# Optimization experiments

Measured on AMD Instinct MI355X. Metric: run time of the kernel, lower is better.

## Reference

```python
import jax, jax.numpy as jnp
import numpy as np

NU = 500000   # num user nodes
NI = 100000   # num item nodes
F  = 300      # item feature dim
D  = 64       # hidden channels
E  = 2000000  # num rated edges
EL = 1000000  # num supervision (label) edges


def setup_inputs() -> dict:
    key = jax.random.key(0)
    ks = jax.random.split(key, 24)
    def nrm(k, shp, scale=0.05):
        return jax.random.normal(k, shp, dtype=jnp.float32) * scale
    inp = {
        "user_emb_w": nrm(ks[0], (NU, D)),
        "item_x": jax.random.normal(ks[1], (NI, F), dtype=jnp.float32),
        "item_lin_w": nrm(ks[2], (F, D)),
        "item_lin_b": jnp.zeros((D,), jnp.float32),
        "Wl1_ui": nrm(ks[3], (D, D)), "Wr1_ui": nrm(ks[4], (D, D)), "b1_ui": jnp.zeros((D,), jnp.float32),
        "Wl1_iu": nrm(ks[5], (D, D)), "Wr1_iu": nrm(ks[6], (D, D)), "b1_iu": jnp.zeros((D,), jnp.float32),
        "Wl2_ui": nrm(ks[7], (D, D)), "Wr2_ui": nrm(ks[8], (D, D)), "b2_ui": jnp.zeros((D,), jnp.float32),
        "Wl2_iu": nrm(ks[9], (D, D)), "Wr2_iu": nrm(ks[10], (D, D)), "b2_iu": jnp.zeros((D,), jnp.float32),
        "user_node_id": jnp.arange(NU, dtype=jnp.int32),
        "edge_src": jax.random.randint(ks[11], (E,), 0, NU, dtype=jnp.int32),
        "edge_dst": jax.random.randint(ks[12], (E,), 0, NI, dtype=jnp.int32),
        "label_src": jax.random.randint(ks[13], (EL,), 0, NU, dtype=jnp.int32),
        "label_dst": jax.random.randint(ks[14], (EL,), 0, NI, dtype=jnp.int32),
    }
    return inp


def _seg_mean(x_src, src, dst, n_dst):
    # mean-aggregate source features onto destination nodes (PyG SAGEConv aggr='mean')
    s = jax.ops.segment_sum(x_src[src], dst, num_segments=n_dst)
    c = jax.ops.segment_sum(jnp.ones(src.shape, x_src.dtype), dst, num_segments=n_dst)
    return s / jnp.maximum(c, 1.0)[:, None]


def reference(user_emb_w, item_x, item_lin_w, item_lin_b,
              Wl1_ui, Wr1_ui, b1_ui, Wl1_iu, Wr1_iu, b1_iu,
              Wl2_ui, Wr2_ui, b2_ui, Wl2_iu, Wr2_iu, b2_iu,
              user_node_id, edge_src, edge_dst, label_src, label_dst):
    # input layers: user embedding lookup, item linear projection
    x_user = user_emb_w[user_node_id]                 # [NU, D]
    x_item = item_x @ item_lin_w + item_lin_b         # [NI, D]

    def hetero_sage(xu, xi, Wl_ui, Wr_ui, bui, Wl_iu, Wr_iu, biu):
        # edge type (user, rates, item): aggregate user msgs at items
        hi = _seg_mean(xu, edge_src, edge_dst, NI) @ Wl_ui + bui + xi @ Wr_ui
        # edge type (item, rev_rates, user): aggregate item msgs at users
        hu = _seg_mean(xi, edge_dst, edge_src, NU) @ Wl_iu + biu + xu @ Wr_iu
        return hu, hi

    hu, hi = hetero_sage(x_user, x_item, Wl1_ui, Wr1_ui, b1_ui, Wl1_iu, Wr1_iu, b1_iu)
    hu, hi = jax.nn.relu(hu), jax.nn.relu(hi)
    hu, hi = hetero_sage(hu, hi, Wl2_ui, Wr2_ui, b2_ui, Wl2_iu, Wr2_iu, b2_iu)

    # DOT predictor on edge_label_index pairs
    return jnp.sum(hu[label_src] * hi[label_dst], axis=-1)   # [EL]
```

## Files before the change

kernel.cpp:

```cpp
#include <hip/hip_runtime.h>

#define NUu 500000
#define NIi 100000
#define FDIM 300
#define DDIM 64
#define NEe 2000000
#define ELl 1000000
#define EMAX (NEe - 1)

#define BSZL_I 8
#define BSZL_U 9
#define NB_I 391
#define NB_U 977
#define NBT (NB_I + NB_U)
#define SH_I 19
#define SH_U 17

typedef __attribute__((ext_vector_type(8))) short s8v;
typedef __attribute__((ext_vector_type(4))) short s4v;
typedef __attribute__((ext_vector_type(4))) float f4v;
typedef unsigned short u16;

__device__ __forceinline__ float bf2f(u16 h) {
    union { unsigned u; float f; } x; x.u = ((unsigned)h) << 16; return x.f;
}
__device__ __forceinline__ u16 f2bf(float f) {
    union { float f; unsigned u; } x; x.f = f;
    unsigned u = x.u;
    u += 0x7FFFu + ((u >> 16) & 1u);
    return (u16)(u >> 16);
}

__global__ __launch_bounds__(256) void k_cast_users(const float* __restrict__ ue,
                                                    const int* __restrict__ uid,
                                                    u16* __restrict__ xu) {
    int idx = blockIdx.x * 256 + threadIdx.x;
    int n  = idx >> 4;
    int d0 = (idx & 15) * 4;
    int src = uid[n];
    const float4* p = (const float4*)(ue + (size_t)src * DDIM + d0);
    float4 v = *p;
    s4v o;
    o[0] = (short)f2bf(v.x); o[1] = (short)f2bf(v.y);
    o[2] = (short)f2bf(v.z); o[3] = (short)f2bf(v.w);
    *(s4v*)(xu + (size_t)n * DDIM + d0) = o;
}

__global__ __launch_bounds__(256) void k_cast_w(const float* __restrict__ W,
                                                u16* __restrict__ wbf) {
    int idx = blockIdx.x * 256 + threadIdx.x;
    if (idx >= 2560) return;
    int f = idx >> 6, lane = idx & 63;
    int q = lane >> 4, c = lane & 15;
    int kstep = f >> 2, nb = f & 3;
    u16* dst = wbf + (size_t)idx * 8;
#pragma unroll
    for (int j = 0; j < 8; j++) {
        int k = kstep * 32 + q * 8 + j;
        float v = (k < FDIM) ? W[k * DDIM + nb * 16 + c] : 0.f;
        dst[j] = f2bf(v);
    }
}

__global__ __launch_bounds__(256) void k_cast_w8(
    const float* __restrict__ W0, const float* __restrict__ W1,
    const float* __restrict__ W2, const float* __restrict__ W3,
    const float* __restrict__ W4, const float* __restrict__ W5,
    const float* __restrict__ W6, const float* __restrict__ W7,
    u16* __restrict__ out) {
    int idx = blockIdx.x * 256 + threadIdx.x;
    if (idx >= 4096) return;
    int wm = idx >> 9;
    int s = idx & 511;
    int ks = s >> 8, nb = (s >> 6) & 3, lane = s & 63;
    int q = lane >> 4, c = lane & 15;
    const float* W;
    switch (wm) {
        case 0: W = W0; break; case 1: W = W1; break;
        case 2: W = W2; break; case 3: W = W3; break;
        case 4: W = W4; break; case 5: W = W5; break;
        case 6: W = W6; break; default: W = W7; break;
    }
    u16* dst = out + (size_t)idx * 8;
#pragma unroll
    for (int j = 0; j < 8; j++) {
        int row = ks * 32 + q * 8 + j;
        dst[j] = f2bf(W[row * DDIM + nb * 16 + c]);
    }
}

__global__ __launch_bounds__(256) void k_item_lin2(const float* __restrict__ ix,
                                                   const u16* __restrict__ wbf,
                                                   const float* __restrict__ b,
                                                   u16* __restrict__ xi) {
    __shared__ __align__(16) u16 wl[40 * 64 * 8];
    int tid = threadIdx.x;
    for (int i = tid; i < 2560; i += 256)
        ((f4v*)wl)[i] = ((const f4v*)wbf)[i];
    __syncthreads();

    int lane = tid & 63;
    int q = lane >> 4, c = lane & 15;
    float bv[4];
#pragma unroll
    for (int nb = 0; nb < 4; nb++) bv[nb] = b[nb * 16 + c];

    int w = blockIdx.x * 4 + (tid >> 6);
    int stride = gridDim.x * 4;
    const int NT = NIi / 16;
    for (int t = w; t < NT; t += stride) {
        int row = t * 16 + c;
        const float* xr = ix + (size_t)row * FDIM;
        f4v acc[4];
#pragma unroll
        for (int nb = 0; nb < 4; nb++) {
            acc[nb][0] = bv[nb]; acc[nb][1] = bv[nb];
            acc[nb][2] = bv[nb]; acc[nb][3] = bv[nb];
        }
#pragma unroll
        for (int ks = 0; ks < 10; ks++) {
            s8v a;
            if (ks < 9 || q == 0) {
                float4 v0 = *(const float4*)(xr + ks * 32 + q * 8);
                float4 v1 = *(const float4*)(xr + ks * 32 + q * 8 + 4);
                a[0] = (short)f2bf(v0.x); a[1] = (short)f2bf(v0.y);
                a[2] = (short)f2bf(v0.z); a[3] = (short)f2bf(v0.w);
                a[4] = (short)f2bf(v1.x); a[5] = (short)f2bf(v1.y);
                a[6] = (short)f2bf(v1.z); a[7] = (short)f2bf(v1.w);
            } else {
                float4 v0 = *(const float4*)(xr + 296);
                a[0] = (short)f2bf(v0.x); a[1] = (short)f2bf(v0.y);
                a[2] = (short)f2bf(v0.z); a[3] = (short)f2bf(v0.w);
                a[4] = 0; a[5] = 0; a[6] = 0; a[7] = 0;
            }
#pragma unroll
            for (int nb = 0; nb < 4; nb++) {
                s8v bb = *(const s8v*)(wl + ((size_t)(ks * 4 + nb) * 64 + lane) * 8);
                acc[nb] = __builtin_amdgcn_mfma_f32_16x16x32_bf16(a, bb, acc[nb], 0, 0, 0);
            }
        }
#pragma unroll
        for (int nb = 0; nb < 4; nb++)
#pragma unroll
            for (int r = 0; r < 4; r++)
                xi[(size_t)(t * 16 + q * 4 + r) * DDIM + nb * 16 + c] = f2bf(acc[nb][r]);
    }
}

__global__ __launch_bounds__(256) void k_hist(const int* __restrict__ src,
                                              const int* __restrict__ dst,
                                              int* __restrict__ hist) {
    __shared__ int h[NBT];
    int t = threadIdx.x;
    for (int c = t; c < NBT; c += 256) h[c] = 0;
    __syncthreads();
    int base = blockIdx.x * 2048;
#pragma unroll
    for (int k = 0; k < 8; k++) {
        int e = base + k * 256 + t;
        if (e < NEe) {
            int s = src[e], d = dst[e];
            atomicAdd(&h[d >> BSZL_I], 1);
            atomicAdd(&h[NB_I + (s >> BSZL_U)], 1);
        }
    }
    __syncthreads();
    for (int c = t; c < NBT; c += 256) {
        int n = h[c];
        if (n) atomicAdd(&hist[c], n);
    }
}

__device__ __forceinline__ void scanN(const int* __restrict__ cnt, int n, int total,
                                      int* __restrict__ base, int* __restrict__ frontier,
                                      int* sb) {
    int t = threadIdx.x;
    int v[8]; int s = 0;
#pragma unroll
    for (int i = 0; i < 8; i++) {
        int idx = t * 8 + i;
        v[i] = (idx < n) ? cnt[idx] : 0;
        s += v[i];
    }
    sb[t] = s; __syncthreads();
    for (int o = 1; o < 256; o <<= 1) {
        int a = (t >= o) ? sb[t - o] : 0;
        __syncthreads();
        sb[t] += a;
        __syncthreads();
    }
    int run = sb[t] - s;
#pragma unroll
    for (int i = 0; i < 8; i++) {
        int idx = t * 8 + i;
        if (idx < n) { base[idx] = run; frontier[idx] = run; }
        run += v[i];
    }
    if (t == 0) base[n] = total;
    __syncthreads();
}

__global__ __launch_bounds__(256) void k_bucket_scan(const int* __restrict__ hist,
                                                     int* __restrict__ base_i, int* __restrict__ fr_i,
                                                     int* __restrict__ base_u, int* __restrict__ fr_u,
                                                     int* __restrict__ rpi, int* __restrict__ rpu) {
    __shared__ int sb[256];
    scanN(hist, NB_I, NEe, base_i, fr_i, sb);
    scanN(hist + NB_I, NB_U, NEe, base_u, fr_u, sb);
    if (threadIdx.x == 0) { rpi[NIi] = NEe; rpu[NUu] = NEe; }
}

__global__ __launch_bounds__(256) void k_scatter(const int* __restrict__ src,
                                                 const int* __restrict__ dst,
                                                 int* __restrict__ fr_i, int* __restrict__ fr_u,
                                                 unsigned* __restrict__ scat_i,
                                                 unsigned* __restrict__ scat_u) {
    __shared__ int h[NBT];
    int t = threadIdx.x;
    for (int c = t; c < NBT; c += 256) h[c] = 0;
    __syncthreads();
    int base = blockIdx.x * 2048;
#pragma unroll
    for (int k = 0; k < 8; k++) {
        int e = base + k * 256 + t;
        if (e < NEe) {
            int s = src[e], d = dst[e];
            atomicAdd(&h[d >> BSZL_I], 1);
            atomicAdd(&h[NB_I + (s >> BSZL_U)], 1);
        }
    }
    __syncthreads();
    for (int c = t; c < NBT; c += 256) {
        int n = h[c];
        if (n) {
            int b = (c < NB_I) ? atomicAdd(&fr_i[c], n) : atomicAdd(&fr_u[c - NB_I], n);
            h[c] = b;
        }
    }
    __syncthreads();
#pragma unroll
    for (int k = 0; k < 8; k++) {
        int e = base + k * 256 + t;
        if (e < NEe) {
            int s = src[e], d = dst[e];
            int p = atomicAdd(&h[d >> BSZL_I], 1);
            scat_i[p] = (unsigned)s | ((unsigned)(d & 255) << SH_I);
            int q = atomicAdd(&h[NB_I + (s >> BSZL_U)], 1);
            scat_u[q] = (unsigned)d | ((unsigned)(s & 511) << SH_U);
        }
    }
}

__global__ __launch_bounds__(256) void k_bfill(const unsigned* __restrict__ scat,
                                               const int* __restrict__ base,
                                               int* __restrict__ rp, int* __restrict__ col,
                                               int shift, int bszlog, int ntotal) {
    __shared__ int cnt[512];
    __shared__ int pos[512];
    __shared__ int sb[256];
    int b = blockIdx.x;
    int t = threadIdx.x;
    int e0 = base[b], e1 = base[b + 1];
    int node0 = b << bszlog;
    int bsz = 1 << bszlog;
    unsigned mask = (1u << shift) - 1u;

    for (int c = t; c < bsz; c += 256) cnt[c] = 0;
    __syncthreads();
    for (int e = e0 + t; e < e1; e += 256) {
        unsigned v = scat[e];
        atomicAdd(&cnt[v >> shift], 1);
    }
    __syncthreads();
    int per = bsz >> 8;
    int loc[2]; int ls = 0;
#pragma unroll
    for (int i = 0; i < 2; i++) {
        loc[i] = (i < per) ? cnt[t * per + i] : 0;
        ls += loc[i];
    }
    sb[t] = ls; __syncthreads();
    for (int o = 1; o < 256; o <<= 1) {
        int a = (t >= o) ? sb[t - o] : 0;
        __syncthreads();
        sb[t] += a;
        __syncthreads();
    }
    int run = e0 + sb[t] - ls;
#pragma unroll
    for (int i = 0; i < 2; i++) {
        if (i < per) {
            int idx = t * per + i;
            int node = node0 + idx;
            if (node < ntotal) rp[node] = run;
            pos[idx] = run;
            run += loc[i];
        }
    }
    __syncthreads();
    for (int e = e0 + t; e < e1; e += 256) {
        unsigned v = scat[e];
        int l = v >> shift;
        int p = atomicAdd(&pos[l], 1);
        col[p] = (int)(v & mask);
    }
}

__global__ __launch_bounds__(256) void k_fused(const u16* __restrict__ feat,
                                               const u16* __restrict__ xf,
                                               const u16* __restrict__ wfrag,
                                               const float* __restrict__ bias,
                                               u16* __restrict__ out,
                                               const int* __restrict__ rp,
                                               const int* __restrict__ col,
                                               int ntiles, int relu) {
    __shared__ __align__(16) u16 wsh[8192];
    int tid = threadIdx.x;
    for (int i = tid; i < 1024; i += 256)
        ((f4v*)wsh)[i] = ((const f4v*)wfrag)[i];
    __syncthreads();

    int lane = tid & 63;
    int q = lane >> 4, c = lane & 15;
    int w = blockIdx.x * 4 + (tid >> 6);
    int stride = gridDim.x * 4;
    float bv[4];
#pragma unroll
    for (int nb = 0; nb < 4; nb++) bv[nb] = bias[nb * 16 + c];

    for (int t = w; t < ntiles; t += stride) {
        int node = t * 16 + c;
        int s0 = rp[node], s1 = rp[node + 1];
        int deg = s1 - s0;
        float inv = (deg > 0) ? 1.0f / (float)deg : 0.0f;

        const s8v* px = (const s8v*)(xf + (size_t)node * DDIM + q * 8);
        s8v x0 = px[0], x1 = px[4];

        float accA[8] = {0.f, 0.f, 0.f, 0.f, 0.f, 0.f, 0.f, 0.f};
        float accB[8] = {0.f, 0.f, 0.f, 0.f, 0.f, 0.f, 0.f, 0.f};

        for (int i = 0; __any(i < deg); i += 2) {
            int ia = s0 + i;
            int ea = min(ia, EMAX);
            int eb = min(ia + 1, EMAX);
            int ra = col[ea];
            int rb = col[eb];
            float ma = (i < deg) ? inv : 0.f;
            float mb = (i + 1 < deg) ? inv : 0.f;
            const u16* fa = feat + (size_t)ra * DDIM + q * 8;
            const u16* fb = feat + (size_t)rb * DDIM + q * 8;
            s8v va0 = *(const s8v*)fa;
            s8v va1 = *(const s8v*)(fa + 32);
            s8v vb0 = *(const s8v*)fb;
            s8v vb1 = *(const s8v*)(fb + 32);
#pragma unroll
            for (int j = 0; j < 8; j++) {
                accA[j] = fmaf(ma, bf2f((u16)va0[j]), accA[j]);
                accB[j] = fmaf(ma, bf2f((u16)va1[j]), accB[j]);
                accA[j] = fmaf(mb, bf2f((u16)vb0[j]), accA[j]);
                accB[j] = fmaf(mb, bf2f((u16)vb1[j]), accB[j]);
            }
        }

        s8v a0, a1;
#pragma unroll
        for (int j = 0; j < 8; j++) {
            a0[j] = (short)f2bf(accA[j]);
            a1[j] = (short)f2bf(accB[j]);
        }

        f4v acc[4];
#pragma unroll
        for (int nb = 0; nb < 4; nb++) {
            acc[nb][0] = bv[nb]; acc[nb][1] = bv[nb];
            acc[nb][2] = bv[nb]; acc[nb][3] = bv[nb];
        }

        unsigned lz = (unsigned)lane * 8u;
        asm volatile("" : "+v"(lz));
        const u16* wb = wsh + lz;
#pragma unroll
        for (int nb = 0; nb < 4; nb++) {
            s8v wl0 = *(const s8v*)(wb + nb * 512);
            s8v wl1 = *(const s8v*)(wb + 2048 + nb * 512);
            s8v wr0 = *(const s8v*)(wb + 4096 + nb * 512);
            s8v wr1 = *(const s8v*)(wb + 6144 + nb * 512);
            acc[nb] = __builtin_amdgcn_mfma_f32_16x16x32_bf16(a0, wl0, acc[nb], 0, 0, 0);
            acc[nb] = __builtin_amdgcn_mfma_f32_16x16x32_bf16(a1, wl1, acc[nb], 0, 0, 0);
            acc[nb] = __builtin_amdgcn_mfma_f32_16x16x32_bf16(x0, wr0, acc[nb], 0, 0, 0);
            acc[nb] = __builtin_amdgcn_mfma_f32_16x16x32_bf16(x1, wr1, acc[nb], 0, 0, 0);
        }
#pragma unroll
        for (int nb = 0; nb < 4; nb++)
#pragma unroll
            for (int r = 0; r < 4; r++) {
                float v = acc[nb][r];
                if (relu) v = fmaxf(v, 0.f);
                out[(size_t)(t * 16 + q * 4 + r) * DDIM + nb * 16 + c] = f2bf(v);
            }
    }
}

__global__ __launch_bounds__(256) void k_dot(const u16* __restrict__ hu,
                                             const u16* __restrict__ hi,
                                             const int* __restrict__ ls,
                                             const int* __restrict__ ld,
                                             float* __restrict__ out) {
    int lane = threadIdx.x & 63;
    int sub = lane >> 3, t8 = lane & 7;
    int w = blockIdx.x * 4 + (threadIdx.x >> 6);
    int stride = gridDim.x * 4;
    const int ngroups = ELl / 8;
    for (int g = w; g < ngroups; g += stride) {
        int e = g * 8 + sub;
        int u = ls[e], it = ld[e];
        s8v av = *(const s8v*)(hu + (size_t)u  * DDIM + t8 * 8);
        s8v bv = *(const s8v*)(hi + (size_t)it * DDIM + t8 * 8);
        float s = 0.f;
#pragma unroll
        for (int k = 0; k < 8; k++) s += bf2f((u16)av[k]) * bf2f((u16)bv[k]);
        s += __shfl_xor(s, 4);
        s += __shfl_xor(s, 2);
        s += __shfl_xor(s, 1);
        if (t8 == 0) out[e] = s;
    }
}

extern "C" void kernel_launch(void* const* d_in, const int* in_sizes, int n_in,
                              void* d_out, int out_size, void* d_ws, size_t ws_size,
                              hipStream_t stream) {
    const float* user_emb = (const float*)d_in[0];
    const float* item_x   = (const float*)d_in[1];
    const float* item_w   = (const float*)d_in[2];
    const float* item_b   = (const float*)d_in[3];
    const float* Wl1_ui = (const float*)d_in[4];
    const float* Wr1_ui = (const float*)d_in[5];
    const float* b1_ui  = (const float*)d_in[6];
    const float* Wl1_iu = (const float*)d_in[7];
    const float* Wr1_iu = (const float*)d_in[8];
    const float* b1_iu  = (const float*)d_in[9];
    const float* Wl2_ui = (const float*)d_in[10];
    const float* Wr2_ui = (const float*)d_in[11];
    const float* b2_ui  = (const float*)d_in[12];
    const float* Wl2_iu = (const float*)d_in[13];
    const float* Wr2_iu = (const float*)d_in[14];
    const float* b2_iu  = (const float*)d_in[15];
    const int* uid  = (const int*)d_in[16];
    const int* esrc = (const int*)d_in[17];
    const int* edst = (const int*)d_in[18];
    const int* lsrc = (const int*)d_in[19];
    const int* ldst = (const int*)d_in[20];
    float* out = (float*)d_out;

    char* ws = (char*)d_ws;
    size_t off = 0;
    auto alloc = [&](size_t bytes) -> void* {
        void* p = ws + off;
        off += (bytes + 255) & ~(size_t)255;
        return p;
    };
    u16* xu_b   = (u16*)alloc((size_t)NUu * DDIM * 2);
    u16* hu1_b  = (u16*)alloc((size_t)NUu * DDIM * 2);
    u16* hu2_b  = (u16*)alloc((size_t)NUu * DDIM * 2);
    u16* xi_b   = (u16*)alloc((size_t)NIi * DDIM * 2);
    u16* hi1_b  = (u16*)alloc((size_t)NIi * DDIM * 2);
    u16* hi2_b  = (u16*)alloc((size_t)NIi * DDIM * 2);
    int* coli = (int*)alloc((size_t)NEe * 4);
    int* colu = (int*)alloc((size_t)NEe * 4);
    int* rpi  = (int*)alloc((size_t)(NIi + 1) * 4);
    int* rpu  = (int*)alloc((size_t)(NUu + 1) * 4);
    int* hist   = (int*)alloc((size_t)NBT * 4);
    int* base_i = (int*)alloc((size_t)(NB_I + 1) * 4);
    int* base_u = (int*)alloc((size_t)(NB_U + 1) * 4);
    int* fr_i   = (int*)alloc((size_t)NB_I * 4);
    int* fr_u   = (int*)alloc((size_t)NB_U * 4);
    u16* wbf    = (u16*)alloc((size_t)40 * 64 * 8 * 2);
    u16* wfrag2 = (u16*)alloc((size_t)4 * 8192 * 2);
    unsigned* scat_i = (unsigned*)xu_b;
    unsigned* scat_u = (unsigned*)((char*)xu_b + (size_t)NEe * 4);

    hipMemsetAsync(hist, 0, (size_t)NBT * 4, stream);
    int nchunks = (NEe + 2047) / 2048;
    k_hist<<<nchunks, 256, 0, stream>>>(esrc, edst, hist);
    k_bucket_scan<<<1, 256, 0, stream>>>(hist, base_i, fr_i, base_u, fr_u, rpi, rpu);
    k_scatter<<<nchunks, 256, 0, stream>>>(esrc, edst, fr_i, fr_u, scat_i, scat_u);
    k_bfill<<<NB_I, 256, 0, stream>>>(scat_i, base_i, rpi, coli, SH_I, BSZL_I, NIi);
    k_bfill<<<NB_U, 256, 0, stream>>>(scat_u, base_u, rpu, colu, SH_U, BSZL_U, NUu);

    k_cast_w<<<10, 256, 0, stream>>>(item_w, wbf);
    k_cast_w8<<<16, 256, 0, stream>>>(Wl1_ui, Wr1_ui, Wl1_iu, Wr1_iu,
                                      Wl2_ui, Wr2_ui, Wl2_iu, Wr2_iu, wfrag2);
    k_cast_users<<<NUu * 16 / 256, 256, 0, stream>>>(user_emb, uid, xu_b);
    k_item_lin2<<<512, 256, 0, stream>>>(item_x, wbf, item_b, xi_b);

    const int NT_I = NIi / 16;
    const int NT_U = NUu / 16;

    k_fused<<<512, 256, 0, stream>>>(xu_b, xi_b, wfrag2 + 0 * 8192, b1_ui,
                                     hi1_b, rpi, coli, NT_I, 1);
    k_fused<<<2048, 256, 0, stream>>>(xi_b, xu_b, wfrag2 + 1 * 8192, b1_iu,
                                      hu1_b, rpu, colu, NT_U, 1);
    k_fused<<<512, 256, 0, stream>>>(hu1_b, hi1_b, wfrag2 + 2 * 8192, b2_ui,
                                     hi2_b, rpi, coli, NT_I, 0);
    k_fused<<<2048, 256, 0, stream>>>(hi1_b, hu1_b, wfrag2 + 3 * 8192, b2_iu,
                                      hu2_b, rpu, colu, NT_U, 0);

    k_dot<<<2048, 256, 0, stream>>>(hu2_b, hi2_b, lsrc, ldst, out);
}
```

Baseline: 850.8 us.

## Sort nodes by degree to balance wavefront gather work in fused SAGE kernel

Adds a degree histogram, scan and counting-sort pass so each 16-node tile in the fused aggregation kernel holds nodes of similar degree, reducing divergence in the __any-driven neighbor loop. Outputs are scattered to the original node rows through shuffled node ids. The gather loop is unrolled to four neighbors per iteration with packed bf16 unpacking, and grid sizes for the item kernels are raised. In exchange it adds several small preprocessing kernels, extra index arrays, and non-contiguous stores and self-feature loads.

```diff
diff --git a/kernel.cpp b/kernel.cpp
--- a/kernel.cpp
+++ b/kernel.cpp
@@ -16,9 +16,12 @@
 #define SH_I 19
 #define SH_U 17
 
+#define DBINS 64
+
 typedef __attribute__((ext_vector_type(8))) short s8v;
 typedef __attribute__((ext_vector_type(4))) short s4v;
 typedef __attribute__((ext_vector_type(4))) float f4v;
+typedef __attribute__((ext_vector_type(4))) unsigned u4v;
 typedef unsigned short u16;
 
 __device__ __forceinline__ float bf2f(u16 h) {
@@ -29,6 +32,12 @@
     unsigned u = x.u;
     u += 0x7FFFu + ((u >> 16) & 1u);
     return (u16)(u >> 16);
+}
+__device__ __forceinline__ float lo2f(unsigned u) {
+    union { unsigned x; float f; } c; c.x = u << 16; return c.f;
+}
+__device__ __forceinline__ float hi2f(unsigned u) {
+    union { unsigned x; float f; } c; c.x = u & 0xffff0000u; return c.f;
 }
 
 __global__ __launch_bounds__(256) void k_cast_users(const float* __restrict__ ue,
@@ -306,12 +315,99 @@
     }
 }
 
+__global__ __launch_bounds__(256) void k_dhist(const int* __restrict__ rp,
+                                               int* __restrict__ hist, int n) {
+    __shared__ int h[DBINS];
+    int t = threadIdx.x;
+    if (t < DBINS) h[t] = 0;
+    __syncthreads();
+    int base = blockIdx.x * 2048;
+#pragma unroll
+    for (int k = 0; k < 8; k++) {
+        int i = base + k * 256 + t;
+        if (i < n) {
+            int d = rp[i + 1] - rp[i];
+            atomicAdd(&h[min(d, DBINS - 1)], 1);
+        }
+    }
+    __syncthreads();
+    if (t < DBINS) { int v = h[t]; if (v) atomicAdd(&hist[t], v); }
+}
+
+__global__ void k_dscan2(int* __restrict__ hu, int* __restrict__ hi) {
+    int t = threadIdx.x;
+    int* h = (t < 64) ? hu : hi;
+    int tt = t & 63;
+    int v = h[tt];
+    int s = v;
+#pragma unroll
+    for (int o = 1; o < 64; o <<= 1) {
+        int a = __shfl_up(s, o);
+        if (tt >= o) s += a;
+    }
+    h[tt] = s - v;
+}
+
+__global__ __launch_bounds__(256) void k_dscatter(const int* __restrict__ rp,
+                                                  int* __restrict__ bpos,
+                                                  int* __restrict__ nsort,
+                                                  int* __restrict__ nstart,
+                                                  int* __restrict__ ndeg, int n) {
+    __shared__ int h[DBINS];
+    __shared__ int bb[DBINS];
+    int t = threadIdx.x;
+    if (t < DBINS) h[t] = 0;
+    __syncthreads();
+    int base = blockIdx.x * 2048;
+    int d[8], s0[8];
+#pragma unroll
+    for (int k = 0; k < 8; k++) {
+        int i = base + k * 256 + t;
+        if (i < n) {
+            int a = rp[i], b = rp[i + 1];
+            s0[k] = a;
+            d[k] = b - a;
+            atomicAdd(&h[min(d[k], DBINS - 1)], 1);
+        } else d[k] = -1;
+    }
+    __syncthreads();
+    if (t < DBINS) {
+        int v = h[t];
+        bb[t] = v ? atomicAdd(&bpos[t], v) : 0;
+        h[t] = 0;
+    }
+    __syncthreads();
+#pragma unroll
+    for (int k = 0; k < 8; k++) {
+        if (d[k] >= 0) {
+            int bin = min(d[k], DBINS - 1);
+            int p = bb[bin] + atomicAdd(&h[bin], 1);
+            nsort[p] = base + k * 256 + t;
+            nstart[p] = s0[k];
+            ndeg[p] = d[k];
+        }
+    }
+}
+
+__device__ __forceinline__ void acc_pair(float m, u4v v0, u4v v1,
+                                         float* A, float* B) {
+#pragma unroll
+    for (int k = 0; k < 4; k++) {
+        A[2 * k]     = fmaf(m, lo2f(v0[k]), A[2 * k]);
+        A[2 * k + 1] = fmaf(m, hi2f(v0[k]), A[2 * k + 1]);
+        B[2 * k]     = fmaf(m, lo2f(v1[k]), B[2 * k]);
+        B[2 * k + 1] = fmaf(m, hi2f(v1[k]), B[2 * k + 1]);
+    }
+}
+
 __global__ __launch_bounds__(256) void k_fused(const u16* __restrict__ feat,
                                                const u16* __restrict__ xf,
                                                const u16* __restrict__ wfrag,
                                                const float* __restrict__ bias,
                                                u16* __restrict__ out,
-                                               const int* __restrict__ rp,
+                                               const int* __restrict__ nsort,
+                                               const int* __restrict__ nstart,
+                                               const int* __restrict__ ndeg,
                                                const int* __restrict__ col,
                                                int ntiles, int relu) {
     __shared__ __align__(16) u16 wsh[8192];
@@ -329,9 +425,10 @@
     for (int nb = 0; nb < 4; nb++) bv[nb] = bias[nb * 16 + c];
 
     for (int t = w; t < ntiles; t += stride) {
-        int node = t * 16 + c;
-        int s0 = rp[node], s1 = rp[node + 1];
-        int deg = s1 - s0;
+        int idx = t * 16 + c;
+        int node = nsort[idx];
+        int s0 = nstart[idx];
+        int deg = ndeg[idx];
         float inv = (deg > 0) ? 1.0f / (float)deg : 0.0f;
 
         const s8v* px = (const s8v*)(xf + (size_t)node * DDIM + q * 8);
@@ -340,27 +437,29 @@
         float accA[8] = {0.f, 0.f, 0.f, 0.f, 0.f, 0.f, 0.f, 0.f};
         float accB[8] = {0.f, 0.f, 0.f, 0.f, 0.f, 0.f, 0.f, 0.f};
 
-        for (int i = 0; __any(i < deg); i += 2) {
-            int ia = s0 + i;
-            int ea = min(ia, EMAX);
-            int eb = min(ia + 1, EMAX);
-            int ra = col[ea];
-            int rb = col[eb];
-            float ma = (i < deg) ? inv : 0.f;
-            float mb = (i + 1 < deg) ? inv : 0.f;
-            const u16* fa = feat + (size_t)ra * DDIM + q * 8;
-            const u16* fb = feat + (size_t)rb * DDIM + q * 8;
-            s8v va0 = *(const s8v*)fa;
-            s8v va1 = *(const s8v*)(fa + 32);
-            s8v vb0 = *(const s8v*)fb;
-            s8v vb1 = *(const s8v*)(fb + 32);
-#pragma unroll
-            for (int j = 0; j < 8; j++) {
-                accA[j] = fmaf(ma, bf2f((u16)va0[j]), accA[j]);
-                accB[j] = fmaf(ma, bf2f((u16)va1[j]), accB[j]);
-                accA[j] = fmaf(mb, bf2f((u16)vb0[j]), accA[j]);
-                accB[j] = fmaf(mb, bf2f((u16)vb1[j]), accB[j]);
-            }
+        for (int i = 0; __any(i < deg); i += 4) {
+            int b = s0 + i;
+            int e0 = min(b,     EMAX);
+            int e1 = min(b + 1, EMAX);
+            int e2 = min(b + 2, EMAX);
+            int e3 = min(b + 3, EMAX);
+            int r0 = col[e0], r1 = col[e1], r2 = col[e2], r3 = col[e3];
+            float m0 = (i     < deg) ? inv : 0.f;
+            float m1 = (i + 1 < deg) ? inv : 0.f;
+            float m2 = (i + 2 < deg) ? inv : 0.f;
+            float m3 = (i + 3 < deg) ? inv : 0.f;
+            const u4v* f0 = (const u4v*)(feat + (size_t)r0 * DDIM + q * 8);
+            const u4v* f1 = (const u4v*)(feat + (size_t)r1 * DDIM + q * 8);
+            const u4v* f2 = (const u4v*)(feat + (size_t)r2 * DDIM + q * 8);
+            const u4v* f3 = (const u4v*)(feat + (size_t)r3 * DDIM + q * 8);
+            u4v a00 = f0[0], a01 = f0[4];
+            u4v a10 = f1[0], a11 = f1[4];
+            u4v a20 = f2[0], a21 = f2[4];
+            u4v a30 = f3[0], a31 = f3[4];
+            acc_pair(m0, a00, a01, accA, accB);
+            acc_pair(m1, a10, a11, accA, accB);
+            acc_pair(m2, a20, a21, accA, accB);
+            acc_pair(m3, a30, a31, accA, accB);
         }
 
         s8v a0, a1;
@@ -391,13 +490,19 @@
             acc[nb] = __builtin_amdgcn_mfma_f32_16x16x32_bf16(x0, wr0, acc[nb], 0, 0, 0);
             acc[nb] = __builtin_amdgcn_mfma_f32_16x16x32_bf16(x1, wr1, acc[nb], 0, 0, 0);
         }
+
+        int rn[4];
+        rn[0] = __shfl(node, q * 4 + 0);
+        rn[1] = __shfl(node, q * 4 + 1);
+        rn[2] = __shfl(node, q * 4 + 2);
+        rn[3] = __shfl(node, q * 4 + 3);
 #pragma unroll
         for (int nb = 0; nb < 4; nb++)
 #pragma unroll
             for (int r = 0; r < 4; r++) {
                 float v = acc[nb][r];
                 if (relu) v = fmaxf(v, 0.f);
-                out[(size_t)(t * 16 + q * 4 + r) * DDIM + nb * 16 + c] = f2bf(v);
+                out[(size_t)rn[r] * DDIM + nb * 16 + c] = f2bf(v);
             }
     }
 }
@@ -477,10 +582,20 @@
     int* fr_u   = (int*)alloc((size_t)NB_U * 4);
     u16* wbf    = (u16*)alloc((size_t)40 * 64 * 8 * 2);
     u16* wfrag2 = (u16*)alloc((size_t)4 * 8192 * 2);
+    int* nsort_i  = (int*)alloc((size_t)NIi * 4);
+    int* nstart_i = (int*)alloc((size_t)NIi * 4);
+    int* ndeg_i   = (int*)alloc((size_t)NIi * 4);
+    int* nsort_u  = (int*)alloc((size_t)NUu * 4);
+    int* nstart_u = (int*)alloc((size_t)NUu * 4);
+    int* ndeg_u   = (int*)alloc((size_t)NUu * 4);
+    int* dhist_i  = (int*)alloc((size_t)DBINS * 4);
+    int* dhist_u  = (int*)alloc((size_t)DBINS * 4);
     unsigned* scat_i = (unsigned*)xu_b;
     unsigned* scat_u = (unsigned*)((char*)xu_b + (size_t)NEe * 4);
 
     hipMemsetAsync(hist, 0, (size_t)NBT * 4, stream);
+    hipMemsetAsync(dhist_i, 0, (size_t)DBINS * 4, stream);
+    hipMemsetAsync(dhist_u, 0, (size_t)DBINS * 4, stream);
     int nchunks = (NEe + 2047) / 2048;
     k_hist<<<nchunks, 256, 0, stream>>>(esrc, edst, hist);
     k_bucket_scan<<<1, 256, 0, stream>>>(hist, base_i, fr_i, base_u, fr_u, rpi, rpu);
@@ -488,23 +603,31 @@
     k_bfill<<<NB_I, 256, 0, stream>>>(scat_i, base_i, rpi, coli, SH_I, BSZL_I, NIi);
     k_bfill<<<NB_U, 256, 0, stream>>>(scat_u, base_u, rpu, colu, SH_U, BSZL_U, NUu);
 
+    int nci = (NIi + 2047) / 2048;
+    int ncu = (NUu + 2047) / 2048;
+    k_dhist<<<nci, 256, 0, stream>>>(rpi, dhist_i, NIi);
+    k_dhist<<<ncu, 256, 0, stream>>>(rpu, dhist_u, NUu);
+    k_dscan2<<<1, 128, 0, stream>>>(dhist_u, dhist_i);
+    k_dscatter<<<nci, 256, 0, stream>>>(rpi, dhist_i, nsort_i, nstart_i, ndeg_i, NIi);
+    k_dscatter<<<ncu, 256, 0, stream>>>(rpu, dhist_u, nsort_u, nstart_u, ndeg_u, NUu);
+
     k_cast_w<<<10, 256, 0, stream>>>(item_w, wbf);
     k_cast_w8<<<16, 256, 0, stream>>>(Wl1_ui, Wr1_ui, Wl1_iu, Wr1_iu,
                                       Wl2_ui, Wr2_ui, Wl2_iu, Wr2_iu, wfrag2);
     k_cast_users<<<NUu * 16 / 256, 256, 0, stream>>>(user_emb, uid, xu_b);
-    k_item_lin2<<<512, 256, 0, stream>>>(item_x, wbf, item_b, xi_b);
+    k_item_lin2<<<1024, 256, 0, stream>>>(item_x, wbf, item_b, xi_b);
 
     const int NT_I = NIi / 16;
     const int NT_U = NUu / 16;
 
-    k_fused<<<512, 256, 0, stream>>>(xu_b, xi_b, wfrag2 + 0 * 8192, b1_ui,
-                                     hi1_b, rpi, coli, NT_I, 1);
+    k_fused<<<1568, 256, 0, stream>>>(xu_b, xi_b, wfrag2 + 0 * 8192, b1_ui,
+                                      hi1_b, nsort_i, nstart_i, ndeg_i, coli, NT_I, 1);
     k_fused<<<2048, 256, 0, stream>>>(xi_b, xu_b, wfrag2 + 1 * 8192, b1_iu,
-                                      hu1_b, rpu, colu, NT_U, 1);
-    k_fused<<<512, 256, 0, stream>>>(hu1_b, hi1_b, wfrag2 + 2 * 8192, b2_ui,
-                                     hi2_b, rpi, coli, NT_I, 0);
+                                      hu1_b, nsort_u, nstart_u, ndeg_u, colu, NT_U, 1);
+    k_fused<<<1568, 256, 0, stream>>>(hu1_b, hi1_b, wfrag2 + 2 * 8192, b2_ui,
+                                      hi2_b, nsort_i, nstart_i, ndeg_i, coli, NT_I, 0);
     k_fused<<<2048, 256, 0, stream>>>(hi1_b, hu1_b, wfrag2 + 3 * 8192, b2_iu,
-                                      hu2_b, rpu, colu, NT_U, 0);
+                                      hu2_b, nsort_u, nstart_u, ndeg_u, colu, NT_U, 0);
 
     k_dot<<<2048, 256, 0, stream>>>(hu2_b, hi2_b, lsrc, ldst, out);
 }
```

New measurement: 813.5 us. 4.4% less time.
